# Performance work log

Measured on AMD Instinct MI355X. Metric: run time of the kernel, lower is better.

Reference implementation:

```python
import jax, jax.numpy as jnp
import numpy as np


def _pairwise_l2(x):
    # x: [N, D] -> [N, N] Euclidean distances, matching (x_i - x_j).norm(dim=-1)
    sq = jnp.sum(x * x, axis=-1)                      # [N]
    sqd = sq[:, None] + sq[None, :] - 2.0 * (x @ x.T)  # [N, N] squared distances
    sqd = jnp.maximum(sqd, 0.0)
    # safe sqrt: zero distance (diagonal) -> 0 with zero gradient, matching
    # torch's norm subgradient at 0
    pos = sqd > 0.0
    return jnp.where(pos, jnp.sqrt(jnp.where(pos, sqd, 1.0)), 0.0)


def setup_inputs() -> dict:
    key = jax.random.key(0)
    data = jax.random.normal(key, (8192, 256), dtype=jnp.float32)
    return {"data": data}


def reference(data) -> jnp.ndarray:
    x = data.reshape(data.shape[0], -1)               # [N, D]
    dist = _pairwise_l2(x)                            # [N, N]
    denom = jax.lax.stop_gradient(jnp.sum(dist, axis=1, keepdims=True))
    return dist / denom
```

## Files before the change

### kernel.cpp

```cpp
#include <hip/hip_runtime.h>
#include <stdint.h>

#define NN 8192
#define DD 256

typedef __attribute__((ext_vector_type(8))) short short8;
typedef __attribute__((ext_vector_type(4))) float f32x4;

typedef const uint32_t __attribute__((address_space(1)))* gbl_ptr_t;
typedef uint32_t __attribute__((address_space(3)))* lds_ptr_t;

__device__ __forceinline__ void gl_lds16(const void* g, const void* l) {
    __builtin_amdgcn_global_load_lds((gbl_ptr_t)(uintptr_t)g,
                                     (lds_ptr_t)(uintptr_t)l, 16, 0, 0);
}

__device__ __forceinline__ unsigned short f32_to_bf16(float f) {
    uint32_t u = __float_as_uint(f);
    u += 0x7fff + ((u >> 16) & 1);
    return (unsigned short)(u >> 16);
}
__device__ __forceinline__ float bf16_to_f32(unsigned short h) {
    return __uint_as_float(((uint32_t)h) << 16);
}

__global__ void prep_kernel(const float* __restrict__ x,
                            unsigned short* __restrict__ hi,
                            unsigned short* __restrict__ lo,
                            float* __restrict__ sq,
                            float* __restrict__ denom) {
    const int r = blockIdx.x;
    const int t = threadIdx.x;
    float v = x[(size_t)r * DD + t];
    unsigned short h = f32_to_bf16(v);
    unsigned short l = f32_to_bf16(v - bf16_to_f32(h));
    int csw = (t & ~63) | ((((t >> 3) & 7) ^ (r & 7)) << 3) | (t & 7);
    hi[(size_t)r * DD + csw] = h;
    lo[(size_t)r * DD + csw] = l;

    float s = v * v;
    #pragma unroll
    for (int m = 32; m >= 1; m >>= 1) s += __shfl_xor(s, m, 64);
    __shared__ float ws[4];
    if ((t & 63) == 0) ws[t >> 6] = s;
    __syncthreads();
    if (t == 0) {
        sq[r] = ws[0] + ws[1] + ws[2] + ws[3];
        denom[r] = 0.0f;
    }
}

__launch_bounds__(256, 2)
__global__ void dist_kernel(const unsigned short* __restrict__ hi,
                            const unsigned short* __restrict__ lo,
                            const float* __restrict__ sq,
                            float* __restrict__ out,
                            float* __restrict__ denom) {
    __shared__ __align__(16) unsigned short lds[4 * 128 * 64];
    unsigned short* ldsAhi = lds;
    unsigned short* ldsAlo = lds + 8192;
    unsigned short* ldsBhi = lds + 16384;
    unsigned short* ldsBlo = lds + 24576;

    const int tid  = threadIdx.x;
    const int lane = tid & 63;
    const int wid  = tid >> 6;
    const int wm = wid >> 1, wn = wid & 1;
    const int l15 = lane & 15, lk = lane >> 4;

    int t = blockIdx.x, bi = 0;
    while (t >= 64 - bi) { t -= 64 - bi; ++bi; }
    const int bj = bi + t;
    const int row0 = bi * 128;
    const int col0 = bj * 128;
    const bool offdiag = (bj > bi);

    f32x4 acc[4][4];
    #pragma unroll
    for (int a = 0; a < 4; ++a)
        #pragma unroll
        for (int b = 0; b < 4; ++b) acc[a][b] = (f32x4){0.f, 0.f, 0.f, 0.f};

    float rsq[4][4], csq[4];
    #pragma unroll
    for (int fm = 0; fm < 4; ++fm)
        #pragma unroll
        for (int r = 0; r < 4; ++r)
            rsq[fm][r] = sq[row0 + wm * 64 + fm * 16 + lk * 4 + r];
    #pragma unroll
    for (int fn = 0; fn < 4; ++fn)
        csq[fn] = sq[col0 + wn * 64 + fn * 16 + l15];

    for (int kt = 0; kt < 4; ++kt) {
        #pragma unroll
        for (int c = 0; c < 4; ++c) {
            int lin  = c * 256 + tid;
            int row  = lin >> 3;
            int col8 = lin & 7;
            size_t goffA = (size_t)(row0 + row) * DD + kt * 64 + col8 * 8;
            size_t goffB = (size_t)(col0 + row) * DD + kt * 64 + col8 * 8;
            size_t lbyte = (size_t)(c * 256 + wid * 64) * 16;
            gl_lds16(hi + goffA, (const char*)ldsAhi + lbyte);
            gl_lds16(lo + goffA, (const char*)ldsAlo + lbyte);
            gl_lds16(hi + goffB, (const char*)ldsBhi + lbyte);
            gl_lds16(lo + goffB, (const char*)ldsBlo + lbyte);
        }
        __syncthreads();

        #pragma unroll
        for (int ks = 0; ks < 2; ++ks) {
            short8 ah[4], al[4], bh[4], bl[4];
            #pragma unroll
            for (int fm = 0; fm < 4; ++fm) {
                int row = wm * 64 + fm * 16 + l15;
                int cb  = (ks * 64 + lk * 16) ^ ((row & 7) << 4);
                int off = row * 64 + (cb >> 1);
                ah[fm] = *(const short8*)(ldsAhi + off);
                al[fm] = *(const short8*)(ldsAlo + off);
            }
            #pragma unroll
            for (int fn = 0; fn < 4; ++fn) {
                int row = wn * 64 + fn * 16 + l15;
                int cb  = (ks * 64 + lk * 16) ^ ((row & 7) << 4);
                int off = row * 64 + (cb >> 1);
                bh[fn] = *(const short8*)(ldsBhi + off);
                bl[fn] = *(const short8*)(ldsBlo + off);
            }
            #pragma unroll
            for (int fm = 0; fm < 4; ++fm)
                #pragma unroll
                for (int fn = 0; fn < 4; ++fn) {
                    acc[fm][fn] = __builtin_amdgcn_mfma_f32_16x16x32_bf16(
                        ah[fm], bh[fn], acc[fm][fn], 0, 0, 0);
                    acc[fm][fn] = __builtin_amdgcn_mfma_f32_16x16x32_bf16(
                        ah[fm], bl[fn], acc[fm][fn], 0, 0, 0);
                    acc[fm][fn] = __builtin_amdgcn_mfma_f32_16x16x32_bf16(
                        al[fm], bh[fn], acc[fm][fn], 0, 0, 0);
                }
        }
        __syncthreads();
    }

    float rp[4][4], cp[4];
    #pragma unroll
    for (int a = 0; a < 4; ++a) {
        cp[a] = 0.f;
        #pragma unroll
        for (int b = 0; b < 4; ++b) rp[a][b] = 0.f;
    }
    float* ldsT = reinterpret_cast<float*>(lds);

    #pragma unroll
    for (int fm = 0; fm < 4; ++fm) {
        #pragma unroll
        for (int fn = 0; fn < 4; ++fn) {
            #pragma unroll
            for (int r = 0; r < 4; ++r) {
                float dot = acc[fm][fn][r];
                float sqd = rsq[fm][r] + csq[fn] - 2.0f * dot;
                sqd = fmaxf(sqd, 0.0f);
                float d = sqrtf(sqd);
                int lr = wm * 64 + fm * 16 + lk * 4 + r;
                int lc = wn * 64 + fn * 16 + l15;
                out[(size_t)(row0 + lr) * NN + col0 + lc] = d;
                rp[fm][r] += d;
                if (offdiag) {
                    cp[fn] += d;
                    ldsT[lc * 128 + (lr ^ ((lc & 31) ^ ((lc & 4) << 2)))] = d;
                }
            }
        }
    }

    #pragma unroll
    for (int fm = 0; fm < 4; ++fm)
        #pragma unroll
        for (int r = 0; r < 4; ++r) {
            float v = rp[fm][r];
            v += __shfl_xor(v, 1, 64);
            v += __shfl_xor(v, 2, 64);
            v += __shfl_xor(v, 4, 64);
            v += __shfl_xor(v, 8, 64);
            if (l15 == 0)
                atomicAdd(&denom[row0 + wm * 64 + fm * 16 + lk * 4 + r], v);
        }

    if (offdiag) {
        #pragma unroll
        for (int fn = 0; fn < 4; ++fn) {
            float v = cp[fn];
            v += __shfl_xor(v, 16, 64);
            v += __shfl_xor(v, 32, 64);
            if (lane < 16)
                atomicAdd(&denom[col0 + wn * 64 + fn * 16 + l15], v);
        }
        __syncthreads();
        #pragma unroll
        for (int it = 0; it < 64; ++it) {
            int idx = it * 256 + tid;
            int c  = idx >> 7;
            int r_ = idx & 127;
            float d = ldsT[c * 128 + (r_ ^ ((c & 31) ^ ((c & 4) << 2)))];
            out[(size_t)(col0 + c) * NN + row0 + r_] = d;
        }
    }
}

__global__ void inv_kernel(float* __restrict__ denom) {
    int i = blockIdx.x * 256 + threadIdx.x;
    if (i < NN) denom[i] = 1.0f / denom[i];
}

__global__ void norm_kernel(float* __restrict__ out,
                            const float* __restrict__ inv) {
    const int i0 = blockIdx.x * blockDim.x + threadIdx.x;
    float4* o4 = reinterpret_cast<float4*>(out);
    #pragma unroll
    for (int k = 0; k < 8; ++k) {
        int idx = k * 2097152 + i0;
        float s = inv[idx >> 11];
        float4 v = o4[idx];
        v.x *= s; v.y *= s; v.z *= s; v.w *= s;
        o4[idx] = v;
    }
}

extern "C" void kernel_launch(void* const* d_in, const int* in_sizes, int n_in,
                              void* d_out, int out_size, void* d_ws, size_t ws_size,
                              hipStream_t stream) {
    const float* x = (const float*)d_in[0];
    float* out = (float*)d_out;
    char* ws = (char*)d_ws;
    unsigned short* hi = (unsigned short*)ws;
    unsigned short* lo = (unsigned short*)(ws + (size_t)NN * DD * 2);
    float* sq    = (float*)(ws + (size_t)NN * DD * 4);
    float* denom = (float*)(ws + (size_t)NN * DD * 4 + NN * 4);

    prep_kernel<<<NN, 256, 0, stream>>>(x, hi, lo, sq, denom);
    dist_kernel<<<2080, 256, 0, stream>>>(hi, lo, sq, out, denom);
    inv_kernel<<<32, 256, 0, stream>>>(denom);
    norm_kernel<<<8192, 256, 0, stream>>>(out, denom);
}
```

Measured before the change: 426.6 us.

## Prefetch next K tile into registers during MFMA and fold inversion into norm kernel

The dist kernel now loads the first K tile directly into LDS, then for each later tile issues global loads into registers before the MFMA loop and writes them to LDS after the compute barrier. The aim is to overlap global memory latency with matrix math. The cost is 16 extra short8 registers per thread and an added barrier per stage, which could hurt occupancy under launch_bounds(256,2). Separately, the inv kernel is removed: the norm kernel now runs one block per row and computes the reciprocal itself, saving one launch.

```diff
diff --git a/kernel.cpp b/kernel.cpp
--- a/kernel.cpp
+++ b/kernel.cpp
@@ -91,21 +91,37 @@
     for (int fn = 0; fn < 4; ++fn)
         csq[fn] = sq[col0 + wn * 64 + fn * 16 + l15];
 
+    #pragma unroll
+    for (int c = 0; c < 4; ++c) {
+        int lin  = c * 256 + tid;
+        int row  = lin >> 3;
+        int col8 = lin & 7;
+        size_t goffA = (size_t)(row0 + row) * DD + col8 * 8;
+        size_t goffB = (size_t)(col0 + row) * DD + col8 * 8;
+        size_t lbyte = (size_t)(c * 256 + wid * 64) * 16;
+        gl_lds16(hi + goffA, (const char*)ldsAhi + lbyte);
+        gl_lds16(lo + goffA, (const char*)ldsAlo + lbyte);
+        gl_lds16(hi + goffB, (const char*)ldsBhi + lbyte);
+        gl_lds16(lo + goffB, (const char*)ldsBlo + lbyte);
+    }
+    __syncthreads();
+
     for (int kt = 0; kt < 4; ++kt) {
-        #pragma unroll
-        for (int c = 0; c < 4; ++c) {
-            int lin  = c * 256 + tid;
-            int row  = lin >> 3;
-            int col8 = lin & 7;
-            size_t goffA = (size_t)(row0 + row) * DD + kt * 64 + col8 * 8;
-            size_t goffB = (size_t)(col0 + row) * DD + kt * 64 + col8 * 8;
-            size_t lbyte = (size_t)(c * 256 + wid * 64) * 16;
-            gl_lds16(hi + goffA, (const char*)ldsAhi + lbyte);
-            gl_lds16(lo + goffA, (const char*)ldsAlo + lbyte);
-            gl_lds16(hi + goffB, (const char*)ldsBhi + lbyte);
-            gl_lds16(lo + goffB, (const char*)ldsBlo + lbyte);
-        }
-        __syncthreads();
+        short8 stg[16];
+        if (kt < 3) {
+            #pragma unroll
+            for (int c = 0; c < 4; ++c) {
+                int lin  = c * 256 + tid;
+                int row  = lin >> 3;
+                int col8 = lin & 7;
+                size_t goffA = (size_t)(row0 + row) * DD + (kt + 1) * 64 + col8 * 8;
+                size_t goffB = (size_t)(col0 + row) * DD + (kt + 1) * 64 + col8 * 8;
+                stg[c * 4 + 0] = *(const short8*)(hi + goffA);
+                stg[c * 4 + 1] = *(const short8*)(lo + goffA);
+                stg[c * 4 + 2] = *(const short8*)(hi + goffB);
+                stg[c * 4 + 3] = *(const short8*)(lo + goffB);
+            }
+        }
 
         #pragma unroll
         for (int ks = 0; ks < 2; ++ks) {
@@ -139,6 +155,18 @@
                 }
         }
         __syncthreads();
+
+        if (kt < 3) {
+            #pragma unroll
+            for (int c = 0; c < 4; ++c) {
+                size_t lbyte = (size_t)(c * 256 + wid * 64 + lane) * 16;
+                *(short8*)((char*)ldsAhi + lbyte) = stg[c * 4 + 0];
+                *(short8*)((char*)ldsAlo + lbyte) = stg[c * 4 + 1];
+                *(short8*)((char*)ldsBhi + lbyte) = stg[c * 4 + 2];
+                *(short8*)((char*)ldsBlo + lbyte) = stg[c * 4 + 3];
+            }
+            __syncthreads();
+        }
     }
 
     float rp[4][4], cp[4];
@@ -206,22 +234,16 @@
     }
 }
 
-__global__ void inv_kernel(float* __restrict__ denom) {
-    int i = blockIdx.x * 256 + threadIdx.x;
-    if (i < NN) denom[i] = 1.0f / denom[i];
-}
-
 __global__ void norm_kernel(float* __restrict__ out,
-                            const float* __restrict__ inv) {
-    const int i0 = blockIdx.x * blockDim.x + threadIdx.x;
-    float4* o4 = reinterpret_cast<float4*>(out);
+                            const float* __restrict__ denom) {
+    const int r = blockIdx.x;
+    const float inv = 1.0f / denom[r];
+    float4* o4 = reinterpret_cast<float4*>(out) + (size_t)r * 2048;
     #pragma unroll
     for (int k = 0; k < 8; ++k) {
-        int idx = k * 2097152 + i0;
-        float s = inv[idx >> 11];
-        float4 v = o4[idx];
-        v.x *= s; v.y *= s; v.z *= s; v.w *= s;
-        o4[idx] = v;
+        float4 v = o4[k * 256 + threadIdx.x];
+        v.x *= inv; v.y *= inv; v.z *= inv; v.w *= inv;
+        o4[k * 256 + threadIdx.x] = v;
     }
 }
 
@@ -238,6 +260,5 @@
 
     prep_kernel<<<NN, 256, 0, stream>>>(x, hi, lo, sq, denom);
     dist_kernel<<<2080, 256, 0, stream>>>(hi, lo, sq, out, denom);
-    inv_kernel<<<32, 256, 0, stream>>>(denom);
-    norm_kernel<<<8192, 256, 0, stream>>>(out, denom);
-}
+    norm_kernel<<<NN, 256, 0, stream>>>(out, denom);
+}
```

Result: no change. 421.3 us (-1.3%).

## Recompute distances in a second pass to fuse normalization into output write

Applied to the files above, without the earlier changes.

Splits the distance kernel into a sum-only pass that accumulates row sums without writing the matrix, and a write pass that recomputes the GEMM and writes already-normalized distances. This removes the separate normalization kernel, which reread and rewrote the full N×N output. The cost is running the split-bf16 GEMM twice.

```diff
diff --git a/kernel.cpp b/kernel.cpp
--- a/kernel.cpp
+++ b/kernel.cpp
@@ -50,96 +50,96 @@
     }
 }
 
+#define DIST_KLOOP()                                                          \
+    for (int kt = 0; kt < 4; ++kt) {                                          \
+        _Pragma("unroll")                                                     \
+        for (int c = 0; c < 4; ++c) {                                         \
+            int lin  = c * 256 + tid;                                         \
+            int row  = lin >> 3;                                              \
+            int col8 = lin & 7;                                               \
+            size_t goffA = (size_t)(row0 + row) * DD + kt * 64 + col8 * 8;    \
+            size_t goffB = (size_t)(col0 + row) * DD + kt * 64 + col8 * 8;    \
+            size_t lbyte = (size_t)(c * 256 + wid * 64) * 16;                 \
+            gl_lds16(hi + goffA, (const char*)ldsAhi + lbyte);                \
+            gl_lds16(lo + goffA, (const char*)ldsAlo + lbyte);                \
+            gl_lds16(hi + goffB, (const char*)ldsBhi + lbyte);                \
+            gl_lds16(lo + goffB, (const char*)ldsBlo + lbyte);                \
+        }                                                                     \
+        __syncthreads();                                                      \
+        _Pragma("unroll")                                                     \
+        for (int ks = 0; ks < 2; ++ks) {                                      \
+            short8 ah[4], al[4], bh[4], bl[4];                                \
+            _Pragma("unroll")                                                 \
+            for (int fm = 0; fm < 4; ++fm) {                                  \
+                int row = wm * 64 + fm * 16 + l15;                            \
+                int cb  = (ks * 64 + lk * 16) ^ ((row & 7) << 4);             \
+                int off = row * 64 + (cb >> 1);                               \
+                ah[fm] = *(const short8*)(ldsAhi + off);                      \
+                al[fm] = *(const short8*)(ldsAlo + off);                      \
+            }                                                                 \
+            _Pragma("unroll")                                                 \
+            for (int fn = 0; fn < 4; ++fn) {                                  \
+                int row = wn * 64 + fn * 16 + l15;                            \
+                int cb  = (ks * 64 + lk * 16) ^ ((row & 7) << 4);             \
+                int off = row * 64 + (cb >> 1);                               \
+                bh[fn] = *(const short8*)(ldsBhi + off);                      \
+                bl[fn] = *(const short8*)(ldsBlo + off);                      \
+            }                                                                 \
+            _Pragma("unroll")                                                 \
+            for (int fm = 0; fm < 4; ++fm)                                    \
+                _Pragma("unroll")                                             \
+                for (int fn = 0; fn < 4; ++fn) {                              \
+                    acc[fm][fn] = __builtin_amdgcn_mfma_f32_16x16x32_bf16(    \
+                        ah[fm], bh[fn], acc[fm][fn], 0, 0, 0);                \
+                    acc[fm][fn] = __builtin_amdgcn_mfma_f32_16x16x32_bf16(    \
+                        ah[fm], bl[fn], acc[fm][fn], 0, 0, 0);                \
+                    acc[fm][fn] = __builtin_amdgcn_mfma_f32_16x16x32_bf16(    \
+                        al[fm], bh[fn], acc[fm][fn], 0, 0, 0);                \
+                }                                                             \
+        }                                                                     \
+        __syncthreads();                                                      \
+    }
+
+#define DIST_PROLOG()                                                         \
+    const int tid  = threadIdx.x;                                             \
+    const int lane = tid & 63;                                                \
+    const int wid  = tid >> 6;                                                \
+    const int wm = wid >> 1, wn = wid & 1;                                    \
+    const int l15 = lane & 15, lk = lane >> 4;                                \
+    int t = blockIdx.x, bi = 0;                                               \
+    while (t >= 64 - bi) { t -= 64 - bi; ++bi; }                              \
+    const int bj = bi + t;                                                    \
+    const int row0 = bi * 128;                                                \
+    const int col0 = bj * 128;                                                \
+    const bool offdiag = (bj > bi);                                           \
+    f32x4 acc[4][4];                                                          \
+    _Pragma("unroll")                                                         \
+    for (int a = 0; a < 4; ++a)                                               \
+        _Pragma("unroll")                                                     \
+        for (int b = 0; b < 4; ++b) acc[a][b] = (f32x4){0.f, 0.f, 0.f, 0.f};  \
+    float rsq[4][4], csq[4];                                                  \
+    _Pragma("unroll")                                                         \
+    for (int fm = 0; fm < 4; ++fm)                                            \
+        _Pragma("unroll")                                                     \
+        for (int r = 0; r < 4; ++r)                                           \
+            rsq[fm][r] = sq[row0 + wm * 64 + fm * 16 + lk * 4 + r];           \
+    _Pragma("unroll")                                                         \
+    for (int fn = 0; fn < 4; ++fn)                                            \
+        csq[fn] = sq[col0 + wn * 64 + fn * 16 + l15];
+
 __launch_bounds__(256, 2)
-__global__ void dist_kernel(const unsigned short* __restrict__ hi,
-                            const unsigned short* __restrict__ lo,
-                            const float* __restrict__ sq,
-                            float* __restrict__ out,
-                            float* __restrict__ denom) {
+__global__ void sum_kernel(const unsigned short* __restrict__ hi,
+                           const unsigned short* __restrict__ lo,
+                           const float* __restrict__ sq,
+                           float* __restrict__ denom) {
     __shared__ __align__(16) unsigned short lds[4 * 128 * 64];
     unsigned short* ldsAhi = lds;
     unsigned short* ldsAlo = lds + 8192;
     unsigned short* ldsBhi = lds + 16384;
     unsigned short* ldsBlo = lds + 24576;
 
-    const int tid  = threadIdx.x;
-    const int lane = tid & 63;
-    const int wid  = tid >> 6;
-    const int wm = wid >> 1, wn = wid & 1;
-    const int l15 = lane & 15, lk = lane >> 4;
-
-    int t = blockIdx.x, bi = 0;
-    while (t >= 64 - bi) { t -= 64 - bi; ++bi; }
-    const int bj = bi + t;
-    const int row0 = bi * 128;
-    const int col0 = bj * 128;
-    const bool offdiag = (bj > bi);
-
-    f32x4 acc[4][4];
-    #pragma unroll
-    for (int a = 0; a < 4; ++a)
-        #pragma unroll
-        for (int b = 0; b < 4; ++b) acc[a][b] = (f32x4){0.f, 0.f, 0.f, 0.f};
-
-    float rsq[4][4], csq[4];
-    #pragma unroll
-    for (int fm = 0; fm < 4; ++fm)
-        #pragma unroll
-        for (int r = 0; r < 4; ++r)
-            rsq[fm][r] = sq[row0 + wm * 64 + fm * 16 + lk * 4 + r];
-    #pragma unroll
-    for (int fn = 0; fn < 4; ++fn)
-        csq[fn] = sq[col0 + wn * 64 + fn * 16 + l15];
-
-    for (int kt = 0; kt < 4; ++kt) {
-        #pragma unroll
-        for (int c = 0; c < 4; ++c) {
-            int lin  = c * 256 + tid;
-            int row  = lin >> 3;
-            int col8 = lin & 7;
-            size_t goffA = (size_t)(row0 + row) * DD + kt * 64 + col8 * 8;
-            size_t goffB = (size_t)(col0 + row) * DD + kt * 64 + col8 * 8;
-            size_t lbyte = (size_t)(c * 256 + wid * 64) * 16;
-            gl_lds16(hi + goffA, (const char*)ldsAhi + lbyte);
-            gl_lds16(lo + goffA, (const char*)ldsAlo + lbyte);
-            gl_lds16(hi + goffB, (const char*)ldsBhi + lbyte);
-            gl_lds16(lo + goffB, (const char*)ldsBlo + lbyte);
-        }
-        __syncthreads();
-
-        #pragma unroll
-        for (int ks = 0; ks < 2; ++ks) {
-            short8 ah[4], al[4], bh[4], bl[4];
-            #pragma unroll
-            for (int fm = 0; fm < 4; ++fm) {
-                int row = wm * 64 + fm * 16 + l15;
-                int cb  = (ks * 64 + lk * 16) ^ ((row & 7) << 4);
-                int off = row * 64 + (cb >> 1);
-                ah[fm] = *(const short8*)(ldsAhi + off);
-                al[fm] = *(const short8*)(ldsAlo + off);
-            }
-            #pragma unroll
-            for (int fn = 0; fn < 4; ++fn) {
-                int row = wn * 64 + fn * 16 + l15;
-                int cb  = (ks * 64 + lk * 16) ^ ((row & 7) << 4);
-                int off = row * 64 + (cb >> 1);
-                bh[fn] = *(const short8*)(ldsBhi + off);
-                bl[fn] = *(const short8*)(ldsBlo + off);
-            }
-            #pragma unroll
-            for (int fm = 0; fm < 4; ++fm)
-                #pragma unroll
-                for (int fn = 0; fn < 4; ++fn) {
-                    acc[fm][fn] = __builtin_amdgcn_mfma_f32_16x16x32_bf16(
-                        ah[fm], bh[fn], acc[fm][fn], 0, 0, 0);
-                    acc[fm][fn] = __builtin_amdgcn_mfma_f32_16x16x32_bf16(
-                        ah[fm], bl[fn], acc[fm][fn], 0, 0, 0);
-                    acc[fm][fn] = __builtin_amdgcn_mfma_f32_16x16x32_bf16(
-                        al[fm], bh[fn], acc[fm][fn], 0, 0, 0);
-                }
-        }
-        __syncthreads();
-    }
+    DIST_PROLOG()
+    DIST_KLOOP()
 
     float rp[4][4], cp[4];
     #pragma unroll
@@ -148,29 +148,17 @@
         #pragma unroll
         for (int b = 0; b < 4; ++b) rp[a][b] = 0.f;
     }
-    float* ldsT = reinterpret_cast<float*>(lds);
-
-    #pragma unroll
-    for (int fm = 0; fm < 4; ++fm) {
-        #pragma unroll
-        for (int fn = 0; fn < 4; ++fn) {
+    #pragma unroll
+    for (int fm = 0; fm < 4; ++fm)
+        #pragma unroll
+        for (int fn = 0; fn < 4; ++fn)
             #pragma unroll
             for (int r = 0; r < 4; ++r) {
-                float dot = acc[fm][fn][r];
-                float sqd = rsq[fm][r] + csq[fn] - 2.0f * dot;
-                sqd = fmaxf(sqd, 0.0f);
-                float d = sqrtf(sqd);
-                int lr = wm * 64 + fm * 16 + lk * 4 + r;
-                int lc = wn * 64 + fn * 16 + l15;
-                out[(size_t)(row0 + lr) * NN + col0 + lc] = d;
+                float sqd = rsq[fm][r] + csq[fn] - 2.0f * acc[fm][fn][r];
+                float d = sqrtf(fmaxf(sqd, 0.0f));
                 rp[fm][r] += d;
-                if (offdiag) {
-                    cp[fn] += d;
-                    ldsT[lc * 128 + (lr ^ ((lc & 31) ^ ((lc & 4) << 2)))] = d;
-                }
+                if (offdiag) cp[fn] += d;
             }
-        }
-    }
 
     #pragma unroll
     for (int fm = 0; fm < 4; ++fm)
@@ -184,7 +172,6 @@
             if (l15 == 0)
                 atomicAdd(&denom[row0 + wm * 64 + fm * 16 + lk * 4 + r], v);
         }
-
     if (offdiag) {
         #pragma unroll
         for (int fn = 0; fn < 4; ++fn) {
@@ -194,6 +181,55 @@
             if (lane < 16)
                 atomicAdd(&denom[col0 + wn * 64 + fn * 16 + l15], v);
         }
+    }
+}
+
+__global__ void inv_kernel(float* __restrict__ denom) {
+    int i = blockIdx.x * 256 + threadIdx.x;
+    if (i < NN) denom[i] = 1.0f / denom[i];
+}
+
+__launch_bounds__(256, 2)
+__global__ void write_kernel(const unsigned short* __restrict__ hi,
+                             const unsigned short* __restrict__ lo,
+                             const float* __restrict__ sq,
+                             const float* __restrict__ inv,
+                             float* __restrict__ out) {
+    __shared__ __align__(16) unsigned short lds[4 * 128 * 64];
+    unsigned short* ldsAhi = lds;
+    unsigned short* ldsAlo = lds + 8192;
+    unsigned short* ldsBhi = lds + 16384;
+    unsigned short* ldsBlo = lds + 24576;
+
+    DIST_PROLOG()
+
+    float rinv[4][4];
+    #pragma unroll
+    for (int fm = 0; fm < 4; ++fm)
+        #pragma unroll
+        for (int r = 0; r < 4; ++r)
+            rinv[fm][r] = inv[row0 + wm * 64 + fm * 16 + lk * 4 + r];
+
+    DIST_KLOOP()
+
+    float* ldsT = reinterpret_cast<float*>(lds);
+
+    #pragma unroll
+    for (int fm = 0; fm < 4; ++fm)
+        #pragma unroll
+        for (int fn = 0; fn < 4; ++fn)
+            #pragma unroll
+            for (int r = 0; r < 4; ++r) {
+                float sqd = rsq[fm][r] + csq[fn] - 2.0f * acc[fm][fn][r];
+                float d = sqrtf(fmaxf(sqd, 0.0f));
+                int lr = wm * 64 + fm * 16 + lk * 4 + r;
+                int lc = wn * 64 + fn * 16 + l15;
+                out[(size_t)(row0 + lr) * NN + col0 + lc] = d * rinv[fm][r];
+                if (offdiag)
+                    ldsT[lc * 128 + (lr ^ ((lc & 31) ^ ((lc & 4) << 2)))] = d;
+            }
+
+    if (offdiag) {
         __syncthreads();
         #pragma unroll
         for (int it = 0; it < 64; ++it) {
@@ -201,27 +237,8 @@
             int c  = idx >> 7;
             int r_ = idx & 127;
             float d = ldsT[c * 128 + (r_ ^ ((c & 31) ^ ((c & 4) << 2)))];
-            out[(size_t)(col0 + c) * NN + row0 + r_] = d;
+            out[(size_t)(col0 + c) * NN + row0 + r_] = d * inv[col0 + c];
         }
-    }
-}
-
-__global__ void inv_kernel(float* __restrict__ denom) {
-    int i = blockIdx.x * 256 + threadIdx.x;
-    if (i < NN) denom[i] = 1.0f / denom[i];
-}
-
-__global__ void norm_kernel(float* __restrict__ out,
-                            const float* __restrict__ inv) {
-    const int i0 = blockIdx.x * blockDim.x + threadIdx.x;
-    float4* o4 = reinterpret_cast<float4*>(out);
-    #pragma unroll
-    for (int k = 0; k < 8; ++k) {
-        int idx = k * 2097152 + i0;
-        float s = inv[idx >> 11];
-        float4 v = o4[idx];
-        v.x *= s; v.y *= s; v.z *= s; v.w *= s;
-        o4[idx] = v;
     }
 }
 
@@ -237,7 +254,7 @@
     float* denom = (float*)(ws + (size_t)NN * DD * 4 + NN * 4);
 
     prep_kernel<<<NN, 256, 0, stream>>>(x, hi, lo, sq, denom);
-    dist_kernel<<<2080, 256, 0, stream>>>(hi, lo, sq, out, denom);
+    sum_kernel<<<2080, 256, 0, stream>>>(hi, lo, sq, denom);
     inv_kernel<<<32, 256, 0, stream>>>(denom);
-    norm_kernel<<<8192, 256, 0, stream>>>(out, denom);
-}
+    write_kernel<<<2080, 256, 0, stream>>>(hi, lo, sq, denom, out);
+}
```

After: 425.6 us. About the same (-0.2%).
